# Optimization experiments

Hardware: AMD Instinct MI355X
Metric: run time of the kernel (lower is better)

Reference implementation:

```python
import jax, jax.numpy as jnp
import numpy as np

BSZ = 2          # batch
H_IMG = 180      # BEV height
W_IMG = 180      # BEV width
BLK = 15         # block_size
D = 128          # d_model
NH = 8           # nhead
DH = D // NH     # head dim


def _bn_relu(x, g, b, m, v, eps=1e-5):
    # eval-mode BatchNorm2d followed by ReLU; x is NCHW
    s = g * jax.lax.rsqrt(v + eps)
    return jax.nn.relu((x - m[None, :, None, None]) * s[None, :, None, None]
                       + b[None, :, None, None])


def _split_tokens(x):
    # (B,C,H,W) -> (B*nb, blk*blk, C), block order = (row-block, col-block)
    B, C, H, W = x.shape
    hb, wb = H // BLK, W // BLK
    x = x.reshape(B, C, hb, BLK, wb, BLK)
    x = x.transpose(0, 2, 4, 1, 3, 5)              # (B,hb,wb,C,blk,blk)
    x = x.reshape(B * hb * wb, C, BLK * BLK)
    return x.transpose(0, 2, 1)                    # (B*nb, L, C)


def _merge_tokens(t, B, H, W):
    # (B*nb, L, C) -> (B,C,H,W), inverse of _split_tokens
    hb, wb = H // BLK, W // BLK
    C = t.shape[-1]
    x = t.transpose(0, 2, 1).reshape(B, hb, wb, C, BLK, BLK)
    x = x.transpose(0, 3, 1, 4, 2, 5)              # (B,C,hb,blk,wb,blk)
    return x.reshape(B, C, H, W)


def setup_inputs() -> dict:
    key = jax.random.key(0)
    ks = jax.random.split(key, 16)
    n = lambda i, shp, sc=0.05: jax.random.normal(ks[i], shp, jnp.float32) * sc
    inp = {
        'camera_feat': jax.random.normal(ks[0], (BSZ, 80, H_IMG, W_IMG), jnp.float32),
        'lidar_feat': jax.random.normal(ks[1], (BSZ, 256, H_IMG, W_IMG), jnp.float32),
        'cam_w': n(2, (D, 80)),
        'cam_gamma': jnp.ones((D,), jnp.float32),
        'cam_beta': jnp.zeros((D,), jnp.float32),
        'cam_mean': n(3, (D,)),
        'cam_var': jax.random.uniform(ks[4], (D,), jnp.float32, 0.5, 1.5),
        'lidar_w': n(5, (D, 256)),
        'lidar_gamma': jnp.ones((D,), jnp.float32),
        'lidar_beta': jnp.zeros((D,), jnp.float32),
        'lidar_mean': n(6, (D,)),
        'lidar_var': jax.random.uniform(ks[7], (D,), jnp.float32, 0.5, 1.5),
        'in_proj_w': n(8, (3 * D, D)),
        'in_proj_b': jnp.zeros((3 * D,), jnp.float32),
        'out_proj_w': n(9, (D, D)),
        'out_proj_b': jnp.zeros((D,), jnp.float32),
        'outc_w': n(10, (256, D, 3, 3)),
        'outc_gamma': jnp.ones((256,), jnp.float32),
        'outc_beta': jnp.zeros((256,), jnp.float32),
        'outc_mean': n(11, (256,)),
        'outc_var': jax.random.uniform(ks[12], (256,), jnp.float32, 0.5, 1.5),
    }
    return inp


def reference(camera_feat, lidar_feat,
              cam_w, cam_gamma, cam_beta, cam_mean, cam_var,
              lidar_w, lidar_gamma, lidar_beta, lidar_mean, lidar_var,
              in_proj_w, in_proj_b, out_proj_w, out_proj_b,
              outc_w, outc_gamma, outc_beta, outc_mean, outc_var):
    B, _, H, W = camera_feat.shape
    # 1x1 conv projections + BN + ReLU
    cam_p = _bn_relu(jnp.einsum('bchw,dc->bdhw', camera_feat, cam_w),
                     cam_gamma, cam_beta, cam_mean, cam_var)
    lid_p = _bn_relu(jnp.einsum('bchw,dc->bdhw', lidar_feat, lidar_w),
                     lidar_gamma, lidar_beta, lidar_mean, lidar_var)
    # windowed tokens: (B*nb, L=225, D)
    cam_t = _split_tokens(cam_p)
    lid_t = _split_tokens(lid_p)
    # cross-attention: query=lidar, key/value=camera (torch MHA math)
    wq, wk, wv = in_proj_w[:D], in_proj_w[D:2 * D], in_proj_w[2 * D:]
    bq, bk, bv = in_proj_b[:D], in_proj_b[D:2 * D], in_proj_b[2 * D:]
    BN, L, _ = lid_t.shape
    q = (lid_t @ wq.T + bq).reshape(BN, L, NH, DH).transpose(0, 2, 1, 3)
    k = (cam_t @ wk.T + bk).reshape(BN, L, NH, DH).transpose(0, 2, 1, 3)
    v = (cam_t @ wv.T + bv).reshape(BN, L, NH, DH).transpose(0, 2, 1, 3)
    scores = jnp.einsum('bhqd,bhkd->bhqk', q, k) / jnp.sqrt(jnp.float32(DH))
    attn = jax.nn.softmax(scores, axis=-1)
    ctx = jnp.einsum('bhqk,bhkd->bhqd', attn, v)
    ctx = ctx.transpose(0, 2, 1, 3).reshape(BN, L, D)
    attn_out = ctx @ out_proj_w.T + out_proj_b
    # merge windows back and fuse
    fused = _merge_tokens(attn_out, B, H, W) + lid_p
    # 3x3 conv + BN + ReLU
    y = jax.lax.conv_general_dilated(
        fused, outc_w, window_strides=(1, 1), padding='SAME',
        dimension_numbers=('NCHW', 'OIHW', 'NCHW'))
    return _bn_relu(y, outc_gamma, outc_beta, outc_mean, outc_var)
```

## Files before the change

### kernel.cpp

```cpp
#include <hip/hip_runtime.h>
#include <hip/hip_bf16.h>
#include <cmath>

#define HW      32400
#define WIMG    180
#define DD      128
#define NHEADS  8
#define DHEAD   16
#define LTOK    225
#define PSTRIDE 64928
#define FBROW   188
#define FBH     182
#define FBSZ    ((size_t)FBH * FBROW * 128)
#define QSCALE  0.36067376022224085f

typedef __attribute__((ext_vector_type(8))) short bf16x8;
typedef __attribute__((ext_vector_type(4))) float f32x4;

union U16B { uint4 u; int4 i; bf16x8 v; };

__device__ __forceinline__ bf16x8 ldfrag(const __hip_bfloat16* p, int ld, int lane) {
  return *(const bf16x8*)(p + (size_t)(lane & 15) * ld + ((lane >> 4) << 3));
}

__device__ __forceinline__ float bf2f(unsigned int u) {
  return __uint_as_float(u << 16);
}

__device__ __forceinline__ unsigned short f2bf(float x) {
  unsigned int b = __float_as_uint(x);
  return (unsigned short)((b + 0x7fffu + ((b >> 16) & 1u)) >> 16);
}

__global__ void k_cast(const float* __restrict__ in, __hip_bfloat16* __restrict__ out, int n) {
  int i = blockIdx.x * 256 + threadIdx.x;
  if (i < n) out[i] = __float2bfloat16(in[i]);
}

__global__ void k_prepproj(const float* __restrict__ w, __hip_bfloat16* __restrict__ wb,
                           int C, int Kpad) {
  int i = blockIdx.x * 256 + threadIdx.x;
  if (i >= 128 * Kpad) return;
  int d = i / Kpad, c = i % Kpad;
  wb[i] = (c < C) ? __float2bfloat16(w[d * C + c]) : __float2bfloat16(0.f);
}

__global__ void k_prepw2(const float* __restrict__ cw, __hip_bfloat16* __restrict__ wcb) {
  int i = blockIdx.x * 256 + threadIdx.x;
  if (i >= 294912) return;
  int oc16  = i / 18432;
  int r0    = i % 18432;
  int tap   = r0 / 2048;
  int r1    = r0 % 2048;
  int chunk = r1 / 512;
  int r2    = r1 % 512;
  int lane  = r2 / 8;
  int e     = r2 % 8;
  int oc = oc16 * 16 + (lane & 15);
  int ic = chunk * 32 + (lane >> 4) * 8 + e;
  wcb[i] = __float2bfloat16(cw[(size_t)(oc * 128 + ic) * 9 + tap]);
}

__global__ void k_zero_border(__hip_bfloat16* __restrict__ fbb) {
  int idx = blockIdx.x * 256 + threadIdx.x;
  if (idx >= 2 * 736 * 16) return;
  int b = idx / (736 * 16);
  int r = idx % (736 * 16);
  int px = r >> 4, blk = r & 15;
  int row, col;
  if (px < 188)      { row = 0;            col = px; }
  else if (px < 376) { row = 181;          col = px - 188; }
  else if (px < 556) { row = px - 376 + 1; col = 0; }
  else               { row = px - 556 + 1; col = 181; }
  ((uint4*)(fbb + (size_t)b * FBSZ + ((size_t)row * FBROW + col) * 128))[blk] =
      make_uint4(0u, 0u, 0u, 0u);
}

__global__ void __launch_bounds__(256) k_proj_mfma(
    const float* __restrict__ in, const __hip_bfloat16* __restrict__ wb,
    const float* __restrict__ g, const float* __restrict__ be,
    const float* __restrict__ mu, const float* __restrict__ var,
    __hip_bfloat16* __restrict__ outp, int C, int Kpad) {
  __shared__ __align__(16) __hip_bfloat16 sa[128 * 64];
  int m0 = blockIdx.x * 128;
  int b = blockIdx.z;
  int tid = threadIdx.x, lane = tid & 63, wid = tid >> 6;
  int wm = (wid >> 1) * 64, wn = (wid & 1) * 64;
  const float* inb = in + (size_t)b * C * HW;
  int sp = (tid >> 1) & 127;
  int sc4 = (tid & 1) * 4;
  int gp = m0 + sp;
  bool pok = gp < HW;
  f32x4 acc[4][4] = {};
  for (int kc = 0; kc < Kpad; kc += 64) {
    __syncthreads();
#pragma unroll
    for (int it = 0; it < 8; ++it) {
      int lc = sc4 + it * 8;
      int c = kc + lc;
      unsigned short u[4];
#pragma unroll
      for (int j = 0; j < 4; ++j) {
        float x = (pok && (c + j) < C) ? inb[(size_t)(c + j) * HW + gp] : 0.f;
        u[j] = f2bf(x);
      }
      int blk = (lc >> 3) ^ (sp & 7);
      char* dst = (char*)sa + sp * 128 + blk * 16 + (lc & 7) * 2;
      *(uint2*)dst = make_uint2(((unsigned)u[1] << 16) | u[0],
                                ((unsigned)u[3] << 16) | u[2]);
    }
    __syncthreads();
#pragma unroll
    for (int ks = 0; ks < 2; ++ks) {
      bf16x8 af[4], bfr[4];
#pragma unroll
      for (int i = 0; i < 4; ++i) {
        int pr = wm + i * 16 + (lane & 15);
        int blk = ((ks * 4 + (lane >> 4)) ^ (pr & 7));
        af[i] = *(const bf16x8*)((const char*)sa + pr * 128 + blk * 16);
      }
#pragma unroll
      for (int j = 0; j < 4; ++j)
        bfr[j] = ldfrag(wb + (size_t)(wn + j * 16) * Kpad + kc + ks * 32, Kpad, lane);
#pragma unroll
      for (int i = 0; i < 4; ++i)
#pragma unroll
        for (int j = 0; j < 4; ++j)
          acc[i][j] = __builtin_amdgcn_mfma_f32_16x16x32_bf16(af[i], bfr[j], acc[i][j], 0, 0, 0);
    }
  }
  int col = lane & 15, rq = lane >> 4;
  __hip_bfloat16* ob = outp + (size_t)b * PSTRIDE * 128;
#pragma unroll
  for (int j = 0; j < 4; ++j) {
    int d = wn + j * 16 + col;
    float s = g[d] * rsqrtf(var[d] + 1e-5f);
    float mm = mu[d], bb = be[d];
#pragma unroll
    for (int i = 0; i < 4; ++i) {
#pragma unroll
      for (int r = 0; r < 4; ++r) {
        int m = m0 + wm + i * 16 + rq * 4 + r;
        if (m < HW) {
          float y = (acc[i][j][r] - mm) * s + bb;
          ob[(size_t)m * 128 + d] = __float2bfloat16(fmaxf(y, 0.f));
        }
      }
    }
  }
}

__global__ void __launch_bounds__(256) k_gemm_bias(
    const __hip_bfloat16* __restrict__ A, const __hip_bfloat16* __restrict__ B,
    const float* __restrict__ bias, __hip_bfloat16* __restrict__ out,
    int K, int ldout, float oscale) {
  int m0 = blockIdx.x * 128, n0 = blockIdx.y * 128, b = blockIdx.z;
  int lane = threadIdx.x & 63, wid = threadIdx.x >> 6;
  int wm = (wid >> 1) * 64, wn = (wid & 1) * 64;
  const __hip_bfloat16* Ab = A + (size_t)b * PSTRIDE * K;
  f32x4 acc[4][4] = {};
  for (int kc = 0; kc < K; kc += 32) {
    bf16x8 af[4], bfr[4];
#pragma unroll
    for (int i = 0; i < 4; ++i)
      af[i] = ldfrag(Ab + (size_t)(m0 + wm + i * 16) * K + kc, K, lane);
#pragma unroll
    for (int j = 0; j < 4; ++j)
      bfr[j] = ldfrag(B + (size_t)(n0 + wn + j * 16) * K + kc, K, lane);
#pragma unroll
    for (int i = 0; i < 4; ++i)
#pragma unroll
      for (int j = 0; j < 4; ++j)
        acc[i][j] = __builtin_amdgcn_mfma_f32_16x16x32_bf16(af[i], bfr[j], acc[i][j], 0, 0, 0);
  }
  int col = lane & 15, rq = lane >> 4;
  __hip_bfloat16* ob = out + (size_t)b * PSTRIDE * ldout;
#pragma unroll
  for (int j = 0; j < 4; ++j) {
    int n = n0 + wn + j * 16 + col;
    float bs = bias[n];
#pragma unroll
    for (int i = 0; i < 4; ++i) {
#pragma unroll
      for (int r = 0; r < 4; ++r) {
        int m = m0 + wm + i * 16 + rq * 4 + r;
        if (m < HW) ob[(size_t)m * ldout + n] = __float2bfloat16((acc[i][j][r] + bs) * oscale);
      }
    }
  }
}

__global__ void __launch_bounds__(256) k_attn_mfma(
    const __hip_bfloat16* __restrict__ qc, const __hip_bfloat16* __restrict__ kvb,
    __hip_bfloat16* __restrict__ ctx) {
  __shared__ __align__(16) uint4 Kf[15 * 64];
  __shared__ __align__(16) uint4 Vf[15 * 64];
  __shared__ __align__(16) unsigned short psh[4 * 256];
  int bn = blockIdx.x, hh = blockIdx.y;
  int b = bn / 144, rr = bn % 144, tby = rr / 12, tbx = rr % 12;
  int tid = threadIdx.x;
  int pbase = tby * 15 * WIMG + tbx * 15;
  const __hip_bfloat16* kvbase = kvb + (size_t)b * PSTRIDE * 256 + hh * 16;

  if (tid < 240) {
    int row = tid;
    int ck = row >> 4, q = row & 15;
    uint4 k0 = make_uint4(0, 0, 0, 0), k1 = k0, v0 = k0, v1 = k0;
    if (row < LTOK) {
      int p = pbase + (row / 15) * WIMG + (row % 15);
      const uint4* kp = (const uint4*)(kvbase + (size_t)p * 256);
      k0 = kp[0]; k1 = kp[1];
      v0 = kp[16]; v1 = kp[17];
    }
    uint4 zz = make_uint4(0, 0, 0, 0);
    Kf[ck * 64 + q]      = k0;
    Kf[ck * 64 + 16 + q] = k1;
    Kf[ck * 64 + 32 + q] = zz;
    Kf[ck * 64 + 48 + q] = zz;
    unsigned short vv[16];
    *(uint4*)&vv[0] = v0;
    *(uint4*)&vv[8] = v1;
    int vg = q >> 3, vj = q & 7;
#pragma unroll
    for (int d = 0; d < 16; ++d)
      ((unsigned short*)&Vf[ck * 64 + vg * 16 + d])[vj] = vv[d];
    Vf[ck * 64 + 32 + q] = zz;
    Vf[ck * 64 + 48 + q] = zz;
  }
  __syncthreads();

  int lane = tid & 63, wid = tid >> 6;
  int g = lane >> 4, q15 = lane & 15;
  int wq0 = wid * 64;
  char* pw_base = (char*)psh + wid * 512;
  const bf16x8* KfB = (const bf16x8*)Kf + lane;
  const bf16x8* VfB = (const bf16x8*)Vf + lane;

  bf16x8 qf[4];
#pragma unroll
  for (int i = 0; i < 4; ++i) {
    int q = wq0 + i * 16 + q15;
    int qq = q < LTOK ? q : 0;
    int p = pbase + (qq / 15) * WIMG + (qq % 15);
    U16B u; u.u = make_uint4(0, 0, 0, 0);
    if (g < 2) u.u = *(const uint4*)(qc + ((size_t)b * PSTRIDE + p) * 128 + hh * 16 + g * 8);
    qf[i] = u.v;
  }

  const f32x4 zacc = {};
  float cm[4];
#pragma unroll
  for (int i = 0; i < 4; ++i) cm[i] = -3.0e38f;

#pragma unroll 1
  for (int ck = 0; ck < 15; ++ck) {
    bf16x8 kf = KfB[ck * 64];
#pragma unroll
    for (int i = 0; i < 4; ++i) {
      f32x4 st = __builtin_amdgcn_mfma_f32_16x16x32_bf16(kf, qf[i], zacc, 0, 0, 0);
      cm[i] = fmaxf(cm[i], fmaxf(fmaxf(st[0], st[1]), fmaxf(st[2], st[3])));
    }
  }
#pragma unroll
  for (int i = 0; i < 4; ++i) {
    cm[i] = fmaxf(cm[i], __shfl_xor(cm[i], 16));
    cm[i] = fmaxf(cm[i], __shfl_xor(cm[i], 32));
  }

  float ls[4] = {0.f, 0.f, 0.f, 0.f};
  f32x4 oac[4] = {};
#pragma unroll 1
  for (int ck = 0; ck < 15; ++ck) {
    bf16x8 kf = KfB[ck * 64];
    bf16x8 vf = VfB[ck * 64];
#pragma unroll
    for (int i = 0; i < 4; ++i) {
      f32x4 st = __builtin_amdgcn_mfma_f32_16x16x32_bf16(kf, qf[i], zacc, 0, 0, 0);
      float p0 = exp2f(st[0] - cm[i]);
      float p1 = exp2f(st[1] - cm[i]);
      float p2 = exp2f(st[2] - cm[i]);
      float p3 = exp2f(st[3] - cm[i]);
      if (ck == 14) {
        if (g) p0 = 0.f;
        p1 = 0.f; p2 = 0.f; p3 = 0.f;
      }
      ls[i] += (p0 + p1) + (p2 + p3);
      unsigned w0 = (unsigned)__bfloat16_as_ushort(__float2bfloat16(p0)) |
                    ((unsigned)__bfloat16_as_ushort(__float2bfloat16(p1)) << 16);
      unsigned w1 = (unsigned)__bfloat16_as_ushort(__float2bfloat16(p2)) |
                    ((unsigned)__bfloat16_as_ushort(__float2bfloat16(p3)) << 16);
      *(uint2*)(pw_base + q15 * 32 + g * 8) = make_uint2(w0, w1);
      U16B pu; pu.u = make_uint4(0, 0, 0, 0);
      if (g < 2) pu.u = *(const uint4*)(pw_base + q15 * 32 + g * 16);
      oac[i] = __builtin_amdgcn_mfma_f32_16x16x32_bf16(vf, pu.v, oac[i], 0, 0, 0);
    }
  }
#pragma unroll
  for (int i = 0; i < 4; ++i) {
    ls[i] += __shfl_xor(ls[i], 16);
    ls[i] += __shfl_xor(ls[i], 32);
  }

  __hip_bfloat16* cb = ctx + (size_t)b * PSTRIDE * 128 + hh * 16;
#pragma unroll
  for (int i = 0; i < 4; ++i) {
    float inv = 1.f / ls[i];
    int qo = wq0 + i * 16 + q15;
    if (qo < LTOK) {
      unsigned lo = (unsigned)f2bf(oac[i][0] * inv) | ((unsigned)f2bf(oac[i][1] * inv) << 16);
      unsigned hi = (unsigned)f2bf(oac[i][2] * inv) | ((unsigned)f2bf(oac[i][3] * inv) << 16);
      int p = pbase + (qo / 15) * WIMG + (qo % 15);
      *(uint2*)(cb + (size_t)p * 128 + g * 4) = make_uint2(lo, hi);
    }
  }
}

__global__ void __launch_bounds__(256) k_outproj_mfma(
    const __hip_bfloat16* __restrict__ ctx, const __hip_bfloat16* __restrict__ wob,
    const float* __restrict__ opb, const __hip_bfloat16* __restrict__ lidb,
    __hip_bfloat16* __restrict__ fb) {
  int m0 = blockIdx.x * 128, b = blockIdx.z;
  int lane = threadIdx.x & 63, wid = threadIdx.x >> 6;
  int wm = (wid >> 1) * 64, wn = (wid & 1) * 64;
  const __hip_bfloat16* Ab = ctx + (size_t)b * PSTRIDE * 128;
  f32x4 acc[4][4] = {};
  for (int kc = 0; kc < 128; kc += 32) {
    bf16x8 af[4], bfr[4];
#pragma unroll
    for (int i = 0; i < 4; ++i)
      af[i] = ldfrag(Ab + (size_t)(m0 + wm + i * 16) * 128 + kc, 128, lane);
#pragma unroll
    for (int j = 0; j < 4; ++j)
      bfr[j] = ldfrag(wob + (size_t)(wn + j * 16) * 128 + kc, 128, lane);
#pragma unroll
    for (int i = 0; i < 4; ++i)
#pragma unroll
      for (int j = 0; j < 4; ++j)
        acc[i][j] = __builtin_amdgcn_mfma_f32_16x16x32_bf16(af[i], bfr[j], acc[i][j], 0, 0, 0);
  }
  int col = lane & 15, rq = lane >> 4;
  const __hip_bfloat16* lb = lidb + (size_t)b * PSTRIDE * 128;
  __hip_bfloat16* fbp = fb + (size_t)b * FBSZ;
#pragma unroll
  for (int j = 0; j < 4; ++j) {
    int n = wn + j * 16 + col;
    float bs = opb[n];
#pragma unroll
    for (int i = 0; i < 4; ++i) {
#pragma unroll
      for (int r = 0; r < 4; ++r) {
        int m = m0 + wm + i * 16 + rq * 4 + r;
        if (m < HW) {
          float v = acc[i][j][r] + bs + __bfloat162float(lb[(size_t)m * 128 + n]);
          int hhh = m / WIMG, www = m % WIMG;
          fbp[((size_t)(hhh + 1) * FBROW + (www + 1)) * 128 + n] = __float2bfloat16(v);
        }
      }
    }
  }
}

__global__ void __launch_bounds__(256) k_conv_mfma(
    const __hip_bfloat16* __restrict__ fb, const __hip_bfloat16* __restrict__ wcb,
    const float* __restrict__ g, const float* __restrict__ be,
    const float* __restrict__ mu, const float* __restrict__ var,
    float* __restrict__ out) {
  __shared__ __align__(16) uint4 Asm[2976];
  int bx = blockIdx.x;
  int h = bx / 6, rem = bx % 6;
  int strip = rem >> 1, ocg = rem & 1;
  int w0 = strip * 60;
  int b = blockIdx.z;
  int tid = threadIdx.x, lane = tid & 63, wid = tid >> 6;
  int q15 = lane & 15, kg = lane >> 4;
  int wpx = (wid & 1) * 32;
  const __hip_bfloat16* fbb = fb + (size_t)b * FBSZ;
  const __hip_bfloat16* Bw = wcb + (size_t)(ocg * 8 + (wid >> 1) * 4) * 18432 + lane * 8;

#pragma unroll
  for (int it = 0; it < 12; ++it) {
    int slot = it * 256 + tid;
    if (slot < 2976) {
      int px = slot % 62;
      int rowk = slot / 62;
      int dy = rowk >> 4, kgrp = rowk & 15;
      Asm[slot] = *(const uint4*)(fbb + ((size_t)(h + dy) * FBROW + (w0 + px)) * 128 + kgrp * 8);
    }
  }

#define LOADB(dst, t)                                                          \
  {                                                                            \
    int tap_ = (t) >> 2, ch_ = (t) & 3;                                        \
    _Pragma("unroll") for (int j = 0; j < 4; ++j)                              \
        dst[j] = *(const bf16x8*)(Bw + (size_t)j * 18432 + tap_ * 2048 + ch_ * 512); \
  }

  bf16x8 bp0[4], bp1[4], bp2[4];
  LOADB(bp0, 0);
  LOADB(bp1, 1);
  LOADB(bp2, 2);
  __syncthreads();

  f32x4 acc[2][4] = {};

#define STEP(t, bp)                                                            \
  {                                                                            \
    int tap_ = (t) >> 2, ch_ = (t) & 3;                                        \
    int dy_ = tap_ / 3, dx_ = tap_ % 3;                                        \
    int rowk_ = (dy_ * 16 + ch_ * 4 + kg) * 62;                                \
    bf16x8 af[2];                                                              \
    _Pragma("unroll") for (int i = 0; i < 2; ++i)                              \
        af[i] = *(const bf16x8*)&Asm[rowk_ + wpx + i * 16 + q15 + dx_];        \
    _Pragma("unroll") for (int i = 0; i < 2; ++i)                              \
        _Pragma("unroll") for (int j = 0; j < 4; ++j)                          \
            acc[i][j] = __builtin_amdgcn_mfma_f32_16x16x32_bf16(af[i], bp[j], acc[i][j], 0, 0, 0); \
  }

#pragma unroll
  for (int t = 0; t < 36; t += 3) {
    STEP(t, bp0);
    if (t + 3 < 36) LOADB(bp0, t + 3);
    STEP(t + 1, bp1);
    if (t + 4 < 36) LOADB(bp1, t + 4);
    STEP(t + 2, bp2);
    if (t + 5 < 36) LOADB(bp2, t + 5);
  }
#undef STEP
#undef LOADB

  int ocbase = ocg * 128 + (wid >> 1) * 64;
#pragma unroll
  for (int j = 0; j < 4; ++j) {
    int oc = ocbase + j * 16 + q15;
    float s = g[oc] * rsqrtf(var[oc] + 1e-5f);
    float mm = mu[oc], bb = be[oc];
#pragma unroll
    for (int i = 0; i < 2; ++i) {
      int pxb = wpx + i * 16 + kg * 4;
      if (pxb < 60) {
        float4 o4;
        o4.x = fmaxf((acc[i][j][0] - mm) * s + bb, 0.f);
        o4.y = fmaxf((acc[i][j][1] - mm) * s + bb, 0.f);
        o4.z = fmaxf((acc[i][j][2] - mm) * s + bb, 0.f);
        o4.w = fmaxf((acc[i][j][3] - mm) * s + bb, 0.f);
        *(float4*)(&out[(size_t)(b * 256 + oc) * HW + h * WIMG + w0 + pxb]) = o4;
      }
    }
  }
}

extern "C" void kernel_launch(void* const* d_in, const int* in_sizes, int n_in,
                              void* d_out, int out_size, void* d_ws, size_t ws_size,
                              hipStream_t stream) {
  const float* camera = (const float*)d_in[0];
  const float* lidar  = (const float*)d_in[1];
  const float* cam_w  = (const float*)d_in[2];
  const float* cam_g  = (const float*)d_in[3];
  const float* cam_b  = (const float*)d_in[4];
  const float* cam_m  = (const float*)d_in[5];
  const float* cam_v  = (const float*)d_in[6];
  const float* lid_w  = (const float*)d_in[7];
  const float* lid_g  = (const float*)d_in[8];
  const float* lid_b  = (const float*)d_in[9];
  const float* lid_m  = (const float*)d_in[10];
  const float* lid_v  = (const float*)d_in[11];
  const float* ipw    = (const float*)d_in[12];
  const float* ipb    = (const float*)d_in[13];
  const float* opw    = (const float*)d_in[14];
  const float* opb    = (const float*)d_in[15];
  const float* ocw    = (const float*)d_in[16];
  const float* ocg    = (const float*)d_in[17];
  const float* ocb    = (const float*)d_in[18];
  const float* ocm    = (const float*)d_in[19];
  const float* ocv    = (const float*)d_in[20];

  __hip_bfloat16* ws = (__hip_bfloat16*)d_ws;
  const size_t NP = (size_t)2 * PSTRIDE * 128;
  __hip_bfloat16* cam_bf = ws;
  __hip_bfloat16* lid_bf = ws + NP;
  __hip_bfloat16* qc     = ws + 2 * NP;
  __hip_bfloat16* kvb    = ws + 3 * NP;
  __hip_bfloat16* wipb   = ws + 5 * NP;
  __hip_bfloat16* wob    = wipb + 384 * 128;
  __hip_bfloat16* wcb    = wob + 128 * 128;
  __hip_bfloat16* wcamb  = wcb + 256 * 9 * 128;
  __hip_bfloat16* wlidb  = wcamb + 128 * 128;
  __hip_bfloat16* fbbuf  = cam_bf;

  dim3 blk(256);
  hipLaunchKernelGGL(k_cast, dim3(192), blk, 0, stream, ipw, wipb, 384 * 128);
  hipLaunchKernelGGL(k_cast, dim3(64), blk, 0, stream, opw, wob, 128 * 128);
  hipLaunchKernelGGL(k_prepw2, dim3(1152), blk, 0, stream, ocw, wcb);
  hipLaunchKernelGGL(k_prepproj, dim3(64), blk, 0, stream, cam_w, wcamb, 80, 128);
  hipLaunchKernelGGL(k_prepproj, dim3(128), blk, 0, stream, lid_w, wlidb, 256, 256);
  dim3 gproj(254, 1, 2);
  hipLaunchKernelGGL(k_proj_mfma, gproj, blk, 0, stream,
                     camera, wcamb, cam_g, cam_b, cam_m, cam_v, cam_bf, 80, 128);
  hipLaunchKernelGGL(k_proj_mfma, gproj, blk, 0, stream,
                     lidar, wlidb, lid_g, lid_b, lid_m, lid_v, lid_bf, 256, 256);
  hipLaunchKernelGGL(k_gemm_bias, dim3(254, 1, 2), blk, 0, stream,
                     lid_bf, wipb, ipb, qc, 128, 128, QSCALE);
  hipLaunchKernelGGL(k_gemm_bias, dim3(254, 2, 2), blk, 0, stream,
                     cam_bf, wipb + 128 * 128, ipb + 128, kvb, 128, 256, 1.0f);
  hipLaunchKernelGGL(k_attn_mfma, dim3(288, 8), blk, 0, stream, qc, kvb, qc);
  hipLaunchKernelGGL(k_zero_border, dim3(92), blk, 0, stream, fbbuf);
  hipLaunchKernelGGL(k_outproj_mfma, dim3(254, 1, 2), blk, 0, stream,
                     qc, wob, opb, lid_bf, fbbuf);
  hipLaunchKernelGGL(k_conv_mfma, dim3(1080, 1, 2), blk, 0, stream,
                     fbbuf, wcb, ocg, ocb, ocm, ocv, (float*)d_out);
}
```

Measured before the change: 305.3 us.

## Share conv input tile across all output channels and tighten attention softmax

The conv kernel now runs 512-thread blocks that cover all 256 output channels of a row strip, so the shared-memory input tile is loaded once per strip rather than once per output-channel half. This halves the grid size and the redundant global loads, but raises per-block resource use and may reduce occupancy. In attention, the max subtraction is folded into the MFMA accumulator initialisation, and branchy zero-filled Q/P loads become unconditional loads. The V-transpose stores into LDS are also rotated per row and chunk to cut bank conflicts.

```diff
diff --git a/kernel.cpp b/kernel.cpp
--- a/kernel.cpp
+++ b/kernel.cpp
@@ -222,8 +222,10 @@
     *(uint4*)&vv[8] = v1;
     int vg = q >> 3, vj = q & 7;
 #pragma unroll
-    for (int d = 0; d < 16; ++d)
+    for (int d0 = 0; d0 < 16; ++d0) {
+      int d = (d0 + q + 2 * ck) & 15;
       ((unsigned short*)&Vf[ck * 64 + vg * 16 + d])[vj] = vv[d];
+    }
     Vf[ck * 64 + 32 + q] = zz;
     Vf[ck * 64 + 48 + q] = zz;
   }
@@ -242,8 +244,8 @@
     int q = wq0 + i * 16 + q15;
     int qq = q < LTOK ? q : 0;
     int p = pbase + (qq / 15) * WIMG + (qq % 15);
-    U16B u; u.u = make_uint4(0, 0, 0, 0);
-    if (g < 2) u.u = *(const uint4*)(qc + ((size_t)b * PSTRIDE + p) * 128 + hh * 16 + g * 8);
+    U16B u;
+    u.u = *(const uint4*)(qc + ((size_t)b * PSTRIDE + p) * 128 + hh * 16 + g * 8);
     qf[i] = u.v;
   }
 
@@ -265,6 +267,11 @@
   for (int i = 0; i < 4; ++i) {
     cm[i] = fmaxf(cm[i], __shfl_xor(cm[i], 16));
     cm[i] = fmaxf(cm[i], __shfl_xor(cm[i], 32));
+  }
+  f32x4 ncm[4];
+#pragma unroll
+  for (int i = 0; i < 4; ++i) {
+    ncm[i][0] = -cm[i]; ncm[i][1] = -cm[i]; ncm[i][2] = -cm[i]; ncm[i][3] = -cm[i];
   }
 
   float ls[4] = {0.f, 0.f, 0.f, 0.f};
@@ -275,11 +282,11 @@
     bf16x8 vf = VfB[ck * 64];
 #pragma unroll
     for (int i = 0; i < 4; ++i) {
-      f32x4 st = __builtin_amdgcn_mfma_f32_16x16x32_bf16(kf, qf[i], zacc, 0, 0, 0);
-      float p0 = exp2f(st[0] - cm[i]);
-      float p1 = exp2f(st[1] - cm[i]);
-      float p2 = exp2f(st[2] - cm[i]);
-      float p3 = exp2f(st[3] - cm[i]);
+      f32x4 st = __builtin_amdgcn_mfma_f32_16x16x32_bf16(kf, qf[i], ncm[i], 0, 0, 0);
+      float p0 = exp2f(st[0]);
+      float p1 = exp2f(st[1]);
+      float p2 = exp2f(st[2]);
+      float p3 = exp2f(st[3]);
       if (ck == 14) {
         if (g) p0 = 0.f;
         p1 = 0.f; p2 = 0.f; p3 = 0.f;
@@ -290,8 +297,8 @@
       unsigned w1 = (unsigned)__bfloat16_as_ushort(__float2bfloat16(p2)) |
                     ((unsigned)__bfloat16_as_ushort(__float2bfloat16(p3)) << 16);
       *(uint2*)(pw_base + q15 * 32 + g * 8) = make_uint2(w0, w1);
-      U16B pu; pu.u = make_uint4(0, 0, 0, 0);
-      if (g < 2) pu.u = *(const uint4*)(pw_base + q15 * 32 + g * 16);
+      U16B pu;
+      pu.u = *(const uint4*)(pw_base + q15 * 32 + (g & 1) * 16);
       oac[i] = __builtin_amdgcn_mfma_f32_16x16x32_bf16(vf, pu.v, oac[i], 0, 0, 0);
     }
   }
@@ -360,26 +367,26 @@
   }
 }
 
-__global__ void __launch_bounds__(256) k_conv_mfma(
+__global__ void __launch_bounds__(512) k_conv_mfma(
     const __hip_bfloat16* __restrict__ fb, const __hip_bfloat16* __restrict__ wcb,
     const float* __restrict__ g, const float* __restrict__ be,
     const float* __restrict__ mu, const float* __restrict__ var,
     float* __restrict__ out) {
   __shared__ __align__(16) uint4 Asm[2976];
   int bx = blockIdx.x;
-  int h = bx / 6, rem = bx % 6;
-  int strip = rem >> 1, ocg = rem & 1;
+  int h = bx / 3, strip = bx % 3;
   int w0 = strip * 60;
   int b = blockIdx.z;
   int tid = threadIdx.x, lane = tid & 63, wid = tid >> 6;
   int q15 = lane & 15, kg = lane >> 4;
   int wpx = (wid & 1) * 32;
+  int ocq = wid >> 1;
   const __hip_bfloat16* fbb = fb + (size_t)b * FBSZ;
-  const __hip_bfloat16* Bw = wcb + (size_t)(ocg * 8 + (wid >> 1) * 4) * 18432 + lane * 8;
-
-#pragma unroll
-  for (int it = 0; it < 12; ++it) {
-    int slot = it * 256 + tid;
+  const __hip_bfloat16* Bw = wcb + (size_t)(ocq * 4) * 18432 + lane * 8;
+
+#pragma unroll
+  for (int it = 0; it < 6; ++it) {
+    int slot = it * 512 + tid;
     if (slot < 2976) {
       int px = slot % 62;
       int rowk = slot / 62;
@@ -428,7 +435,7 @@
 #undef STEP
 #undef LOADB
 
-  int ocbase = ocg * 128 + (wid >> 1) * 64;
+  int ocbase = ocq * 64;
 #pragma unroll
   for (int j = 0; j < 4; ++j) {
     int oc = ocbase + j * 16 + q15;
@@ -506,6 +513,6 @@
   hipLaunchKernelGGL(k_zero_border, dim3(92), blk, 0, stream, fbbuf);
   hipLaunchKernelGGL(k_outproj_mfma, dim3(254, 1, 2), blk, 0, stream,
                      qc, wob, opb, lid_bf, fbbuf);
-  hipLaunchKernelGGL(k_conv_mfma, dim3(1080, 1, 2), blk, 0, stream,
+  hipLaunchKernelGGL(k_conv_mfma, dim3(540, 1, 2), dim3(512), 0, stream,
                      fbbuf, wcb, ocg, ocb, ocm, ocv, (float*)d_out);
 }
```

Result: no change. 307.9 us (+0.9%).
